# Kernel tuning notes

Hardware: AMD Instinct MI355X
Metric: run time of the kernel (lower is better)

Reference implementation:

```python
import jax, jax.numpy as jnp
import numpy as np

DIM = 1024
N_HEADS = 16
HEAD_DIM = DIM // N_HEADS
SCALE = HEAD_DIM ** (-0.5)


def setup_inputs() -> dict:
    key = jax.random.key(0)
    ks = jax.random.split(key, 5)
    B, N = 2, 2048
    x = jax.random.normal(ks[0], (B, N, DIM), dtype=jnp.float32)
    # torch nn.Linear weight layout: (out_features, in_features)
    qkv_w = jax.random.normal(ks[1], (3 * DIM, DIM), dtype=jnp.float32) * 0.02
    qkv_b = jax.random.normal(ks[2], (3 * DIM,), dtype=jnp.float32) * 0.02
    proj_w = jax.random.normal(ks[3], (DIM, DIM), dtype=jnp.float32) * 0.02
    proj_b = jax.random.normal(ks[4], (DIM,), dtype=jnp.float32) * 0.02
    return {"x": x, "qkv_w": qkv_w, "qkv_b": qkv_b, "proj_w": proj_w, "proj_b": proj_b}


def reference(x, qkv_w, qkv_b, proj_w, proj_b):
    B, N, C = x.shape
    # QKV projection: (B,N,C) -> (B,N,3C)
    qkv = jnp.einsum('bnc,oc->bno', x, qkv_w) + qkv_b
    # (B,N,3,H,Dh) -> (3,B,H,N,Dh)
    qkv = qkv.reshape(B, N, 3, N_HEADS, HEAD_DIM).transpose(2, 0, 3, 1, 4)
    q, k, v = qkv[0], qkv[1], qkv[2]
    attn = jnp.einsum('bhqd,bhkd->bhqk', q, k) * SCALE
    attn = jax.nn.softmax(attn, axis=-1)
    out = jnp.einsum('bhqk,bhkd->bhqd', attn, v)
    out = out.transpose(0, 2, 1, 3).reshape(B, N, C)  # concat heads
    out = jnp.einsum('bnc,oc->bno', out, proj_w) + proj_b
    return out
```

## Files before the change

kernel.cpp:

```cpp
#include <hip/hip_runtime.h>

#define DIM 1024
#define NHEADS 16
#define HD 64
#define NSEQ 2048
#define MROWS 4096
#define QKV_LD 3072

typedef __attribute__((ext_vector_type(8))) short short8;
typedef __attribute__((ext_vector_type(4))) short short4v;
typedef __attribute__((ext_vector_type(4))) float f32x4;

typedef __attribute__((address_space(1))) void gvoid_t;
typedef __attribute__((address_space(3))) void lvoid_t;

#if __has_builtin(__builtin_amdgcn_exp2f)
#define EXP2(x) __builtin_amdgcn_exp2f(x)
#else
#define EXP2(x) exp2f(x)
#endif

#if __has_builtin(__builtin_amdgcn_mfma_f32_16x16x16_bf16)
#define MFMA16(a, b, c) __builtin_amdgcn_mfma_f32_16x16x16_bf16(a, b, c, 0, 0, 0)
#elif __has_builtin(__builtin_amdgcn_mfma_f32_16x16x16bf16_1k)
#define MFMA16(a, b, c) __builtin_amdgcn_mfma_f32_16x16x16bf16_1k(a, b, c, 0, 0, 0)
#else
static __device__ __forceinline__ f32x4 mfma16_asm(short4v a, short4v b, f32x4 c) {
  __asm__("v_mfma_f32_16x16x16_bf16 %0, %1, %2, %0" : "+v"(c) : "v"(a), "v"(b));
  return c;
}
#define MFMA16(a, b, c) mfma16_asm(a, b, c)
#endif

#define EXP_SCALE 0.18033688011112042f

__device__ __forceinline__ unsigned short f2bf(float f) {
  unsigned int u = __builtin_bit_cast(unsigned int, f);
  u += 0x7FFFu + ((u >> 16) & 1u);
  return (unsigned short)(u >> 16);
}

__device__ __forceinline__ void gl_lds16(const void* g, void* l) {
  __builtin_amdgcn_global_load_lds((gvoid_t*)g, (lvoid_t*)l, 16, 0, 0);
}

__global__ __launch_bounds__(256) void cast_bf16_3(
    const float* __restrict__ x, const float* __restrict__ wq,
    const float* __restrict__ wp,
    unsigned short* __restrict__ xb, unsigned short* __restrict__ wqb,
    unsigned short* __restrict__ wpb)
{
  int g = blockIdx.x * 256 + threadIdx.x;
  const float* src;
  unsigned short* dst;
  if (g < 1048576)            { src = x  + (size_t)g * 4;              dst = xb  + (size_t)g * 4; }
  else if (g < 1048576 + 786432) { int t = g - 1048576; src = wq + (size_t)t * 4; dst = wqb + (size_t)t * 4; }
  else                        { int t = g - 1048576 - 786432; src = wp + (size_t)t * 4; dst = wpb + (size_t)t * 4; }
  float4 v = *(const float4*)src;
  ushort4 o;
  o.x = f2bf(v.x); o.y = f2bf(v.y); o.z = f2bf(v.z); o.w = f2bf(v.w);
  *(ushort4*)dst = o;
}

__global__ __launch_bounds__(256) void gemm_nt(
    const unsigned short* __restrict__ A,
    const unsigned short* __restrict__ Bw,
    const float* __restrict__ bias,
    int K, int mode,
    unsigned short* __restrict__ oq,
    unsigned short* __restrict__ ovt,
    float* __restrict__ of)
{
  __shared__ unsigned short As[128 * 64];
  __shared__ unsigned short Bs[128 * 64];

  const int tid  = threadIdx.x;
  const int wave = tid >> 6, lane = tid & 63;
  const int quad = lane >> 4, l15 = lane & 15;
  const int mblk = blockIdx.x * 128;
  const int nblk = blockIdx.y * 128;
  const int wrow = (wave >> 1) * 64, wcol = (wave & 1) * 64;

  f32x4 acc[4][4] = {};

  const int sr8 = lane >> 3;
  const int sp8 = lane & 7;
  const int qc  = sp8 ^ sr8;
  const unsigned short* aB = A  + (size_t)(mblk + wave * 32 + sr8) * K + qc * 8;
  const unsigned short* bB = Bw + (size_t)(nblk + wave * 32 + sr8) * K + qc * 8;

  for (int k0 = 0; k0 < K; k0 += 64) {
    __syncthreads();
#pragma unroll
    for (int i = 0; i < 4; ++i) {
      gl_lds16(aB + (size_t)(i * 8) * K + k0, As + (wave * 32 + i * 8) * 64);
      gl_lds16(bB + (size_t)(i * 8) * K + k0, Bs + (wave * 32 + i * 8) * 64);
    }
    asm volatile("s_waitcnt vmcnt(0)" ::: "memory");
    __syncthreads();

#pragma unroll
    for (int ks = 0; ks < 2; ++ks) {
      short8 af[4], bf8[4];
#pragma unroll
      for (int mt = 0; mt < 4; ++mt) {
        int row = wrow + mt * 16 + l15;
        af[mt] = *(const short8*)(As + row * 64 + (((ks * 4 + quad) ^ (row & 7)) * 8));
      }
#pragma unroll
      for (int nt = 0; nt < 4; ++nt) {
        int row = wcol + nt * 16 + l15;
        bf8[nt] = *(const short8*)(Bs + row * 64 + (((ks * 4 + quad) ^ (row & 7)) * 8));
      }
#pragma unroll
      for (int mt = 0; mt < 4; ++mt)
#pragma unroll
        for (int nt = 0; nt < 4; ++nt)
          acc[mt][nt] = __builtin_amdgcn_mfma_f32_16x16x32_bf16(af[mt], bf8[nt], acc[mt][nt], 0, 0, 0);
    }
  }

  float bv[4];
#pragma unroll
  for (int nt = 0; nt < 4; ++nt) bv[nt] = bias[nblk + wcol + nt * 16 + l15];

  if (mode == 0) {
#pragma unroll
    for (int mt = 0; mt < 4; ++mt) {
      int row0 = mblk + wrow + mt * 16 + quad * 4;
#pragma unroll
      for (int nt = 0; nt < 4; ++nt) {
        int col = nblk + wcol + nt * 16 + l15;
#pragma unroll
        for (int r = 0; r < 4; ++r)
          of[(size_t)(row0 + r) * DIM + col] = acc[mt][nt][r] + bv[nt];
      }
    }
  } else if (nblk < 2048) {
    const float qs = (nblk < 1024) ? EXP_SCALE : 1.0f;
#pragma unroll
    for (int mt = 0; mt < 4; ++mt) {
      int row0 = mblk + wrow + mt * 16 + quad * 4;
#pragma unroll
      for (int nt = 0; nt < 4; ++nt) {
        int col = nblk + wcol + nt * 16 + l15;
#pragma unroll
        for (int r = 0; r < 4; ++r)
          oq[(size_t)(row0 + r) * QKV_LD + col] = f2bf((acc[mt][nt][r] + bv[nt]) * qs);
      }
    }
  } else {
#pragma unroll
    for (int mt = 0; mt < 4; ++mt) {
      int row0 = mblk + wrow + mt * 16 + quad * 4;
      int n0 = row0 & (NSEQ - 1);
      int bb = row0 >> 11;
      int tt  = n0 >> 6;
      int kin = n0 & 63;
      int kt  = kin >> 4;
      int qv  = (kin >> 2) & 3;
#pragma unroll
      for (int nt = 0; nt < 4; ++nt) {
        int colr = (nblk - 2048) + wcol + nt * 16 + l15;
        int bh = bb * NHEADS + (colr >> 6);
        int d  = colr & 63;
        int dt = d >> 4, dl15 = d & 15;
        ushort4 pk;
        pk.x = f2bf(acc[mt][nt][0] + bv[nt]);
        pk.y = f2bf(acc[mt][nt][1] + bv[nt]);
        pk.z = f2bf(acc[mt][nt][2] + bv[nt]);
        pk.w = f2bf(acc[mt][nt][3] + bv[nt]);
        size_t off = (size_t)(bh * 32 + tt) * 4096 + kt * 1024 + (dt >> 1) * 512
                   + qv * 128 + dl15 * 8 + (dt & 1) * 4;
        *(ushort4*)(ovt + off) = pk;
      }
    }
  }
}

__global__ __launch_bounds__(256) void gemm_nt64(
    const unsigned short* __restrict__ A,
    const unsigned short* __restrict__ Bw,
    const float* __restrict__ bias,
    int K,
    float* __restrict__ of)
{
  __shared__ unsigned short As[64 * 64];
  __shared__ unsigned short Bs[128 * 64];

  const int tid  = threadIdx.x;
  const int wave = tid >> 6, lane = tid & 63;
  const int quad = lane >> 4, l15 = lane & 15;
  const int mblk = blockIdx.x * 64;
  const int nblk = blockIdx.y * 128;
  const int wrow = (wave >> 1) * 32, wcol = (wave & 1) * 64;

  f32x4 acc[2][4] = {};

  const int sr8 = lane >> 3;
  const int sp8 = lane & 7;
  const int qc  = sp8 ^ sr8;
  const unsigned short* aB = A  + (size_t)(mblk + wave * 16 + sr8) * K + qc * 8;
  const unsigned short* bB = Bw + (size_t)(nblk + wave * 32 + sr8) * K + qc * 8;

  for (int k0 = 0; k0 < K; k0 += 64) {
    __syncthreads();
    gl_lds16(aB + k0,                 As + (wave * 16) * 64);
    gl_lds16(aB + (size_t)8 * K + k0, As + (wave * 16 + 8) * 64);
#pragma unroll
    for (int i = 0; i < 4; ++i)
      gl_lds16(bB + (size_t)(i * 8) * K + k0, Bs + (wave * 32 + i * 8) * 64);
    asm volatile("s_waitcnt vmcnt(0)" ::: "memory");
    __syncthreads();

#pragma unroll
    for (int ks = 0; ks < 2; ++ks) {
      short8 af[2], bf8[4];
#pragma unroll
      for (int mt = 0; mt < 2; ++mt) {
        int row = wrow + mt * 16 + l15;
        af[mt] = *(const short8*)(As + row * 64 + (((ks * 4 + quad) ^ (row & 7)) * 8));
      }
#pragma unroll
      for (int nt = 0; nt < 4; ++nt) {
        int row = wcol + nt * 16 + l15;
        bf8[nt] = *(const short8*)(Bs + row * 64 + (((ks * 4 + quad) ^ (row & 7)) * 8));
      }
#pragma unroll
      for (int mt = 0; mt < 2; ++mt)
#pragma unroll
        for (int nt = 0; nt < 4; ++nt)
          acc[mt][nt] = __builtin_amdgcn_mfma_f32_16x16x32_bf16(af[mt], bf8[nt], acc[mt][nt], 0, 0, 0);
    }
  }

  float bv[4];
#pragma unroll
  for (int nt = 0; nt < 4; ++nt) bv[nt] = bias[nblk + wcol + nt * 16 + l15];

#pragma unroll
  for (int mt = 0; mt < 2; ++mt) {
    int row0 = mblk + wrow + mt * 16 + quad * 4;
#pragma unroll
    for (int nt = 0; nt < 4; ++nt) {
      int col = nblk + wcol + nt * 16 + l15;
#pragma unroll
      for (int r = 0; r < 4; ++r)
        of[(size_t)(row0 + r) * DIM + col] = acc[mt][nt][r] + bv[nt];
    }
  }
}

__global__ __launch_bounds__(256, 4) void attn_fused(
    const unsigned short* __restrict__ qkv,
    const unsigned short* __restrict__ vfrag,
    unsigned short* __restrict__ aout)
{
  __shared__ unsigned short Ks[2][64 * 64];
  __shared__ unsigned short Vs[2][64 * 64];

  const int tid  = threadIdx.x;
  const int wave = tid >> 6, lane = tid & 63;
  const int quad = lane >> 4, l15 = lane & 15;
  const int qh = wave & 1;
  const int kh = wave >> 1;
  const int bh = blockIdx.x, b = bh >> 4, h = bh & 15;
  const int q0 = blockIdx.y * 64;
  const size_t qkvB = (size_t)b * NSEQ * QKV_LD;

  short8 qf[2][2];
#pragma unroll
  for (int nq = 0; nq < 2; ++nq)
#pragma unroll
    for (int ks = 0; ks < 2; ++ks)
      qf[nq][ks] = *(const short8*)(qkv + qkvB +
          (size_t)(q0 + qh * 32 + nq * 16 + l15) * QKV_LD + h * HD + ks * 32 + quad * 8);

  f32x4 oacc[4][2] = {};
  float lsum[2] = {0.f, 0.f};

  const int sr8 = lane >> 3;
  const int sp8 = lane & 7;

  const int r0s = wave * 16 + sr8;
  const int r1s = wave * 16 + 8 + sr8;
  const int qc0 = sp8 ^ (r0s & 7);
  const int qc1 = sp8 ^ (r1s & 7);
  const unsigned short* kBase = qkv + qkvB + DIM + h * HD;
  const unsigned short* kSrc0 = kBase + (size_t)r0s * QKV_LD + qc0 * 8;
  const unsigned short* kSrc1 = kBase + (size_t)r1s * QKV_LD + qc1 * 8;
  const unsigned short* vfT = vfrag + (size_t)bh * 32 * 4096 + wave * 512 + lane * 8;

  auto stage = [&](int bufi, int kkn) {
    gl_lds16(kSrc0 + (size_t)kkn * QKV_LD, &Ks[bufi][(wave * 16) * 64]);
    gl_lds16(kSrc1 + (size_t)kkn * QKV_LD, &Ks[bufi][(wave * 16 + 8) * 64]);
    const unsigned short* vs = vfT + (size_t)(kkn >> 6) * 4096;
    gl_lds16(vs,        &Vs[bufi][wave * 512]);
    gl_lds16(vs + 2048, &Vs[bufi][wave * 512 + 2048]);
  };

  stage(0, 0);
  asm volatile("s_waitcnt vmcnt(0)" ::: "memory");
  __syncthreads();

  for (int kk = 0; kk < NSEQ; kk += 64) {
    const int cur = (kk >> 6) & 1;
    if (kk + 64 < NSEQ) stage(cur ^ 1, kk + 64);

    const unsigned short* Kc = &Ks[cur][0];
    const unsigned short* Vc = &Vs[cur][0];

    short8 kf[2][2];
#pragma unroll
    for (int kt = 0; kt < 2; ++kt)
#pragma unroll
      for (int ks = 0; ks < 2; ++ks) {
        int row = kh * 32 + kt * 16 + l15;
        kf[kt][ks] = *(const short8*)(Kc + row * 64 + (((ks * 4 + quad) ^ (row & 7)) * 8));
      }

    f32x4 sacc[2][2] = {};
    __builtin_amdgcn_s_setprio(1);
#pragma unroll
    for (int kt = 0; kt < 2; ++kt)
#pragma unroll
      for (int nq = 0; nq < 2; ++nq) {
        sacc[kt][nq] = __builtin_amdgcn_mfma_f32_16x16x32_bf16(kf[kt][0], qf[nq][0], sacc[kt][nq], 0, 0, 0);
        sacc[kt][nq] = __builtin_amdgcn_mfma_f32_16x16x32_bf16(kf[kt][1], qf[nq][1], sacc[kt][nq], 0, 0, 0);
      }
    __builtin_amdgcn_s_setprio(0);

    short4v vf[4][2];
#pragma unroll
    for (int kt = 0; kt < 2; ++kt)
#pragma unroll
      for (int p = 0; p < 2; ++p) {
        short8 vv = *(const short8*)(Vc + (kh * 2 + kt) * 1024 + p * 512 + lane * 8);
        vf[2 * p    ][kt] = __builtin_shufflevector(vv, vv, 0, 1, 2, 3);
        vf[2 * p + 1][kt] = __builtin_shufflevector(vv, vv, 4, 5, 6, 7);
      }

#pragma unroll
    for (int kt = 0; kt < 2; ++kt)
#pragma unroll
      for (int nq = 0; nq < 2; ++nq) {
        float p0 = EXP2(sacc[kt][nq][0]);
        float p1 = EXP2(sacc[kt][nq][1]);
        float p2 = EXP2(sacc[kt][nq][2]);
        float p3 = EXP2(sacc[kt][nq][3]);
        lsum[nq] += (p0 + p1) + (p2 + p3);
        unsigned r0 = __builtin_bit_cast(unsigned, p0) + 0x8000u;
        unsigned r1 = __builtin_bit_cast(unsigned, p1) + 0x8000u;
        unsigned r2 = __builtin_bit_cast(unsigned, p2) + 0x8000u;
        unsigned r3 = __builtin_bit_cast(unsigned, p3) + 0x8000u;
        uint2 pd;
        pd.x = __builtin_amdgcn_perm(r1, r0, 0x07060302u);
        pd.y = __builtin_amdgcn_perm(r3, r2, 0x07060302u);
        short4v pf = __builtin_bit_cast(short4v, pd);
        __builtin_amdgcn_s_setprio(1);
#pragma unroll
        for (int dt = 0; dt < 4; ++dt)
          oacc[dt][nq] = MFMA16(vf[dt][kt], pf, oacc[dt][nq]);
        __builtin_amdgcn_s_setprio(0);
      }

    asm volatile("s_waitcnt vmcnt(0)" ::: "memory");
    __syncthreads();
  }

#pragma unroll
  for (int nq = 0; nq < 2; ++nq) {
    lsum[nq] += __shfl_xor(lsum[nq], 16);
    lsum[nq] += __shfl_xor(lsum[nq], 32);
  }

  {
    float* red0 = (float*)&Ks[0][0];
    float* red1 = (float*)&Vs[0][0];
    float* red = qh ? red1 : red0;
    const int base = lane * 34;
    if (kh == 1) {
#pragma unroll
      for (int dt = 0; dt < 4; ++dt)
#pragma unroll
        for (int nq = 0; nq < 2; ++nq)
#pragma unroll
          for (int r = 0; r < 4; ++r)
            red[base + dt * 8 + nq * 4 + r] = oacc[dt][nq][r];
      red[base + 32] = lsum[0];
      red[base + 33] = lsum[1];
    }
    __syncthreads();
    if (kh == 0) {
#pragma unroll
      for (int dt = 0; dt < 4; ++dt)
#pragma unroll
        for (int nq = 0; nq < 2; ++nq)
#pragma unroll
          for (int r = 0; r < 4; ++r)
            oacc[dt][nq][r] += red[base + dt * 8 + nq * 4 + r];
      lsum[0] += red[base + 32];
      lsum[1] += red[base + 33];

      const size_t outB = (size_t)(b * NSEQ + q0 + qh * 32) * DIM + h * HD;
#pragma unroll
      for (int nq = 0; nq < 2; ++nq) {
        float inv = 1.0f / lsum[nq];
        const size_t rowB = outB + (size_t)(nq * 16 + l15) * DIM;
#pragma unroll
        for (int dt = 0; dt < 4; ++dt) {
          unsigned a0 = __builtin_bit_cast(unsigned, oacc[dt][nq][0] * inv) + 0x8000u;
          unsigned a1 = __builtin_bit_cast(unsigned, oacc[dt][nq][1] * inv) + 0x8000u;
          unsigned a2 = __builtin_bit_cast(unsigned, oacc[dt][nq][2] * inv) + 0x8000u;
          unsigned a3 = __builtin_bit_cast(unsigned, oacc[dt][nq][3] * inv) + 0x8000u;
          uint2 st;
          st.x = __builtin_amdgcn_perm(a1, a0, 0x07060302u);
          st.y = __builtin_amdgcn_perm(a3, a2, 0x07060302u);
          *(uint2*)(aout + rowB + dt * 16 + quad * 4) = st;
        }
      }
    }
  }
}

extern "C" void kernel_launch(void* const* d_in, const int* in_sizes, int n_in,
                              void* d_out, int out_size, void* d_ws, size_t ws_size,
                              hipStream_t stream) {
  (void)in_sizes; (void)n_in; (void)out_size; (void)ws_size;
  const float* x      = (const float*)d_in[0];
  const float* qkv_w  = (const float*)d_in[1];
  const float* qkv_b  = (const float*)d_in[2];
  const float* proj_w = (const float*)d_in[3];
  const float* proj_b = (const float*)d_in[4];
  float* out = (float*)d_out;

  char* ws = (char*)d_ws;
  unsigned short* xb   = (unsigned short*)(ws);
  unsigned short* wqb  = (unsigned short*)(ws + ( 8u << 20));
  unsigned short* wpb  = (unsigned short*)(ws + (14u << 20));
  unsigned short* qkv  = (unsigned short*)(ws + (16u << 20));
  unsigned short* vtw  = (unsigned short*)(ws + (40u << 20));
  unsigned short* attn = (unsigned short*)(ws + (48u << 20));

  cast_bf16_3<<<8192, 256, 0, stream>>>(x, qkv_w, proj_w, xb, wqb, wpb);
  gemm_nt<<<dim3(32, 24), 256, 0, stream>>>(xb, wqb, qkv_b, DIM, 1, qkv, vtw, nullptr);
  attn_fused<<<dim3(32, 32), 256, 0, stream>>>(qkv, vtw, attn);
  gemm_nt64<<<dim3(64, 8), 256, 0, stream>>>(attn, wpb, proj_b, DIM, out);
}
```

Baseline: 181.2 us.

## Use 16x16x32 MFMA for PV product with permuted K rows and V layout

The P·V product switches from 16x16x16 bf16 MFMA to 16x16x32 MFMA, which halves the number of PV matrix instructions. To make this work, the K rows loaded per lane are permuted so that the QK^T accumulator registers line up with the 32-wide k operand. The V fragment layout written by the QKV GEMM is rearranged to match, and the LDS swizzle becomes a new PHI function to avoid bank conflicts under the new row mapping. The risk is correctness, since the K-row permutation, the V layout and the swizzle must all agree exactly.

```diff
diff --git a/kernel.cpp b/kernel.cpp
--- a/kernel.cpp
+++ b/kernel.cpp
@@ -20,19 +20,9 @@
 #define EXP2(x) exp2f(x)
 #endif
 
-#if __has_builtin(__builtin_amdgcn_mfma_f32_16x16x16_bf16)
-#define MFMA16(a, b, c) __builtin_amdgcn_mfma_f32_16x16x16_bf16(a, b, c, 0, 0, 0)
-#elif __has_builtin(__builtin_amdgcn_mfma_f32_16x16x16bf16_1k)
-#define MFMA16(a, b, c) __builtin_amdgcn_mfma_f32_16x16x16bf16_1k(a, b, c, 0, 0, 0)
-#else
-static __device__ __forceinline__ f32x4 mfma16_asm(short4v a, short4v b, f32x4 c) {
-  __asm__("v_mfma_f32_16x16x16_bf16 %0, %1, %2, %0" : "+v"(c) : "v"(a), "v"(b));
-  return c;
-}
-#define MFMA16(a, b, c) mfma16_asm(a, b, c)
-#endif
-
 #define EXP_SCALE 0.18033688011112042f
+
+#define PHI(r) (((r) & 7) ^ ((((r) >> 3) & 3) << 1))
 
 __device__ __forceinline__ unsigned short f2bf(float f) {
   unsigned int u = __builtin_bit_cast(unsigned int, f);
@@ -157,8 +147,9 @@
       int bb = row0 >> 11;
       int tt  = n0 >> 6;
       int kin = n0 & 63;
-      int kt  = kin >> 4;
-      int qv  = (kin >> 2) & 3;
+      int g   = kin >> 5;
+      int qv2 = (kin >> 3) & 3;
+      int j0  = kin & 7;
 #pragma unroll
       for (int nt = 0; nt < 4; ++nt) {
         int colr = (nblk - 2048) + wcol + nt * 16 + l15;
@@ -170,8 +161,8 @@
         pk.y = f2bf(acc[mt][nt][1] + bv[nt]);
         pk.z = f2bf(acc[mt][nt][2] + bv[nt]);
         pk.w = f2bf(acc[mt][nt][3] + bv[nt]);
-        size_t off = (size_t)(bh * 32 + tt) * 4096 + kt * 1024 + (dt >> 1) * 512
-                   + qv * 128 + dl15 * 8 + (dt & 1) * 4;
+        size_t off = (size_t)(bh * 32 + tt) * 4096 + g * 2048 + dt * 512
+                   + qv2 * 128 + dl15 * 8 + j0;
         *(ushort4*)(ovt + off) = pk;
       }
     }
@@ -284,12 +275,15 @@
 
   const int r0s = wave * 16 + sr8;
   const int r1s = wave * 16 + 8 + sr8;
-  const int qc0 = sp8 ^ (r0s & 7);
-  const int qc1 = sp8 ^ (r1s & 7);
+  const int qc0 = sp8 ^ PHI(r0s);
+  const int qc1 = sp8 ^ PHI(r1s);
   const unsigned short* kBase = qkv + qkvB + DIM + h * HD;
   const unsigned short* kSrc0 = kBase + (size_t)r0s * QKV_LD + qc0 * 8;
   const unsigned short* kSrc1 = kBase + (size_t)r1s * QKV_LD + qc1 * 8;
   const unsigned short* vfT = vfrag + (size_t)bh * 32 * 4096 + wave * 512 + lane * 8;
+
+  const int prow0 = kh * 32 + ((l15 & ~3) << 1) + (l15 & 3);
+  const int prow1 = prow0 + 4;
 
   auto stage = [&](int bufi, int kkn) {
     gl_lds16(kSrc0 + (size_t)kkn * QKV_LD, &Ks[bufi][(wave * 16) * 64]);
@@ -312,12 +306,10 @@
 
     short8 kf[2][2];
 #pragma unroll
-    for (int kt = 0; kt < 2; ++kt)
-#pragma unroll
-      for (int ks = 0; ks < 2; ++ks) {
-        int row = kh * 32 + kt * 16 + l15;
-        kf[kt][ks] = *(const short8*)(Kc + row * 64 + (((ks * 4 + quad) ^ (row & 7)) * 8));
-      }
+    for (int ks = 0; ks < 2; ++ks) {
+      kf[0][ks] = *(const short8*)(Kc + prow0 * 64 + (((ks * 4 + quad) ^ PHI(prow0)) * 8));
+      kf[1][ks] = *(const short8*)(Kc + prow1 * 64 + (((ks * 4 + quad) ^ PHI(prow1)) * 8));
+    }
 
     f32x4 sacc[2][2] = {};
     __builtin_amdgcn_s_setprio(1);
@@ -330,39 +322,42 @@
       }
     __builtin_amdgcn_s_setprio(0);
 
-    short4v vf[4][2];
-#pragma unroll
-    for (int kt = 0; kt < 2; ++kt)
-#pragma unroll
-      for (int p = 0; p < 2; ++p) {
-        short8 vv = *(const short8*)(Vc + (kh * 2 + kt) * 1024 + p * 512 + lane * 8);
-        vf[2 * p    ][kt] = __builtin_shufflevector(vv, vv, 0, 1, 2, 3);
-        vf[2 * p + 1][kt] = __builtin_shufflevector(vv, vv, 4, 5, 6, 7);
-      }
-
-#pragma unroll
-    for (int kt = 0; kt < 2; ++kt)
-#pragma unroll
-      for (int nq = 0; nq < 2; ++nq) {
-        float p0 = EXP2(sacc[kt][nq][0]);
-        float p1 = EXP2(sacc[kt][nq][1]);
-        float p2 = EXP2(sacc[kt][nq][2]);
-        float p3 = EXP2(sacc[kt][nq][3]);
-        lsum[nq] += (p0 + p1) + (p2 + p3);
-        unsigned r0 = __builtin_bit_cast(unsigned, p0) + 0x8000u;
-        unsigned r1 = __builtin_bit_cast(unsigned, p1) + 0x8000u;
-        unsigned r2 = __builtin_bit_cast(unsigned, p2) + 0x8000u;
-        unsigned r3 = __builtin_bit_cast(unsigned, p3) + 0x8000u;
-        uint2 pd;
-        pd.x = __builtin_amdgcn_perm(r1, r0, 0x07060302u);
-        pd.y = __builtin_amdgcn_perm(r3, r2, 0x07060302u);
-        short4v pf = __builtin_bit_cast(short4v, pd);
-        __builtin_amdgcn_s_setprio(1);
-#pragma unroll
-        for (int dt = 0; dt < 4; ++dt)
-          oacc[dt][nq] = MFMA16(vf[dt][kt], pf, oacc[dt][nq]);
-        __builtin_amdgcn_s_setprio(0);
-      }
+    short8 vf8[4];
+#pragma unroll
+    for (int dt = 0; dt < 4; ++dt)
+      vf8[dt] = *(const short8*)(Vc + kh * 2048 + dt * 512 + lane * 8);
+
+#pragma unroll
+    for (int nq = 0; nq < 2; ++nq) {
+      float p0 = EXP2(sacc[0][nq][0]);
+      float p1 = EXP2(sacc[0][nq][1]);
+      float p2 = EXP2(sacc[0][nq][2]);
+      float p3 = EXP2(sacc[0][nq][3]);
+      float p4 = EXP2(sacc[1][nq][0]);
+      float p5 = EXP2(sacc[1][nq][1]);
+      float p6 = EXP2(sacc[1][nq][2]);
+      float p7 = EXP2(sacc[1][nq][3]);
+      lsum[nq] += ((p0 + p1) + (p2 + p3)) + ((p4 + p5) + (p6 + p7));
+      unsigned r0 = __builtin_bit_cast(unsigned, p0) + 0x8000u;
+      unsigned r1 = __builtin_bit_cast(unsigned, p1) + 0x8000u;
+      unsigned r2 = __builtin_bit_cast(unsigned, p2) + 0x8000u;
+      unsigned r3 = __builtin_bit_cast(unsigned, p3) + 0x8000u;
+      unsigned r4 = __builtin_bit_cast(unsigned, p4) + 0x8000u;
+      unsigned r5 = __builtin_bit_cast(unsigned, p5) + 0x8000u;
+      unsigned r6 = __builtin_bit_cast(unsigned, p6) + 0x8000u;
+      unsigned r7 = __builtin_bit_cast(unsigned, p7) + 0x8000u;
+      uint4 pd;
+      pd.x = __builtin_amdgcn_perm(r1, r0, 0x07060302u);
+      pd.y = __builtin_amdgcn_perm(r3, r2, 0x07060302u);
+      pd.z = __builtin_amdgcn_perm(r5, r4, 0x07060302u);
+      pd.w = __builtin_amdgcn_perm(r7, r6, 0x07060302u);
+      short8 pf = __builtin_bit_cast(short8, pd);
+      __builtin_amdgcn_s_setprio(1);
+#pragma unroll
+      for (int dt = 0; dt < 4; ++dt)
+        oacc[dt][nq] = __builtin_amdgcn_mfma_f32_16x16x32_bf16(vf8[dt], pf, oacc[dt][nq], 0, 0, 0);
+      __builtin_amdgcn_s_setprio(0);
+    }
 
     asm volatile("s_waitcnt vmcnt(0)" ::: "memory");
     __syncthreads();
```

After: 177.9 us, median of 3. About the same (-1.8%).
